# Performance work log

Measured on AMD Instinct MI355X. Metric: run time of the kernel, lower is better.

The kernel has to match this reference:

```python
import jax, jax.numpy as jnp
import numpy as np

NV = 10000
NF = 20000
BATCH = 8


def _make_faces(nv, nf):
    # Synthetic closed-ish mesh connectivity: each vertex touches several faces,
    # guaranteeing every diagonal (degree) entry is > 0.
    i = np.arange(nf)
    half = nf // 2
    f0 = i % nv
    f1 = np.where(i < half, (i + 1) % nv, (i + 3) % nv)
    f2 = np.where(i < half, (i + 2) % nv, (i + 5) % nv)
    return np.stack([f0, f1, f2], axis=1).astype(np.int64)


def _build_laplacian(nv, faces):
    # Faithful replication of LaplacianLoss.__init__ (assignment, not accumulation).
    L = np.zeros((nv, nv), dtype=np.float32)
    f0, f1, f2 = faces[:, 0], faces[:, 1], faces[:, 2]
    L[f0, f1] = -1
    L[f1, f0] = -1
    L[f1, f2] = -1
    L[f2, f1] = -1
    L[f2, f0] = -1
    L[f0, f2] = -1
    r = np.arange(nv)
    L[r, r] = -L.sum(1)  # degree on diagonal
    L /= L[r, r][:, None]  # normalize each row by its diagonal
    return L


def setup_inputs() -> dict:
    key = jax.random.key(0)
    kx, kw = jax.random.split(key)
    faces = _make_faces(NV, NF)
    laplacian = jnp.asarray(_build_laplacian(NV, faces))  # [nv, nv]
    x = jax.random.normal(kx, (BATCH, NV, 3), dtype=jnp.float32)
    vertex_weight = jax.random.uniform(kw, (1,), dtype=jnp.float32) + 0.5
    return {"x": x, "laplacian": laplacian, "vertex_weight": vertex_weight}


def reference(x, laplacian, vertex_weight):
    # lx[b, i, k] = sum_j L[i, j] * x[b, j, k]
    lx = jnp.einsum('ij,bjk->bik', laplacian, x)
    lx = lx * vertex_weight
    # torch.norm over dims (1,2) == Frobenius norm per batch element; scaled by nv
    nv = x.shape[1]
    return jnp.sqrt(jnp.sum(lx * lx, axis=(1, 2))) * nv  # [B]
```

## Files before the change

### kernel.cpp

```cpp
#include <hip/hip_runtime.h>
#include <math.h>


#define NVERT 10000
#define TJ 256
#define NTILES 40
#define TPG 10
#define JG 4
#define RPW 4
#define RPB 16
#define NROWG 625
#define GRID1 (NROWG * JG)
#define GRID2 40

__global__ __launch_bounds__(256, 3) void lap_main(
    const float* __restrict__ x, const float* __restrict__ L,
    float* __restrict__ C) {
  __shared__ __align__(16) float smem[6400];

  const int tid  = threadIdx.x;
  const int lane = tid & 63;
  const int wave = tid >> 6;
  const int rg   = blockIdx.x >> 2;
  const int jg   = blockIdx.x & 3;
  const int row0 = rg * RPB + wave * RPW;

  __align__(16) float acc[RPW][24];
#pragma unroll
  for (int r = 0; r < RPW; ++r)
#pragma unroll
    for (int n = 0; n < 24; ++n) acc[r][n] = 0.f;

  const float4* __restrict__ xg = (const float4*)x;

  for (int tt = 0; tt < TPG; ++tt) {
    const int t = jg * TPG + tt;
    const int jcount = (t == NTILES - 1) ? (NVERT - t * TJ) : TJ;
    __syncthreads();

    const int nf4 = (jcount * 3) >> 2;
    if (tid < nf4) {
#pragma unroll
      for (int b = 0; b < 8; ++b)
        ((float4*)smem)[b * 192 + tid] = xg[b * 7500 + t * 192 + tid];
    }
    __syncthreads();

    const int col0 = t * TJ + 4 * lane;
    if (4 * lane < jcount) {
      __align__(16) float Lv[RPW][4];
#pragma unroll
      for (int r = 0; r < RPW; ++r)
        *(float4*)&Lv[r][0] =
            *(const float4*)(L + (long)(row0 + r) * NVERT + col0);

      const float* xs = smem + 12 * lane;
#pragma unroll
      for (int b = 0; b < 8; ++b) {
        __align__(16) float xv[12];
        *(float4*)&xv[0] = *(const float4*)(xs + b * 768);
        *(float4*)&xv[4] = *(const float4*)(xs + b * 768 + 4);
        *(float4*)&xv[8] = *(const float4*)(xs + b * 768 + 8);
#pragma unroll
        for (int r = 0; r < RPW; ++r)
#pragma unroll
          for (int jj = 0; jj < 4; ++jj)
#pragma unroll
            for (int k = 0; k < 3; ++k)
              acc[r][b * 3 + k] += Lv[r][jj] * xv[jj * 3 + k];
      }
    }
  }

  for (int w = 0; w < 4; ++w) {
    __syncthreads();
    if (wave == w) {
#pragma unroll
      for (int r = 0; r < RPW; ++r)
#pragma unroll
        for (int c = 0; c < 6; ++c)
          *(float4*)&smem[lane * 100 + r * 24 + c * 4] = *(float4*)&acc[r][c * 4];
    }
    __syncthreads();
    if (tid < 96) {
      float s = 0.f;
#pragma unroll
      for (int l = 0; l < 64; ++l) s += smem[l * 100 + tid];
      const int row = rg * RPB + w * RPW + tid / 24;
      atomicAdd(&C[row * 24 + (tid % 24)], s);
    }
  }
}

__global__ __launch_bounds__(256) void lap_reduce(
    const float* __restrict__ C, const float* __restrict__ wv,
    float* __restrict__ out, float* __restrict__ Sg, unsigned* __restrict__ ctr) {
  __shared__ float sS[8];
  const int tid = threadIdx.x;
  if (tid < 8) sS[tid] = 0.f;
  __syncthreads();

  const int row = blockIdx.x * 256 + tid;
  float pb[8] = {0.f, 0.f, 0.f, 0.f, 0.f, 0.f, 0.f, 0.f};
  if (row < NVERT) {
    const float* rp = C + (long)row * 24;
#pragma unroll
    for (int b = 0; b < 8; ++b) {
      float s = 0.f;
#pragma unroll
      for (int k = 0; k < 3; ++k) {
        float v = rp[b * 3 + k];
        s += v * v;
      }
      pb[b] = s;
    }
  }
#pragma unroll
  for (int b = 0; b < 8; ++b) atomicAdd(&sS[b], pb[b]);
  __syncthreads();
  if (tid < 8) atomicAdd(&Sg[tid], sS[tid]);
  __syncthreads();

  if (tid == 0) {
    __threadfence();
    unsigned old = atomicAdd(ctr, 1u);
    if (old == (unsigned)(gridDim.x - 1)) {
      __threadfence();
      const float w = wv[0];
#pragma unroll
      for (int b = 0; b < 8; ++b) {
        float s = atomicAdd(&Sg[b], 0.f);
        out[b] = w * sqrtf(s) * (float)NVERT;
      }
    }
  }
}

extern "C" void kernel_launch(void* const* d_in, const int* in_sizes, int n_in,
                              void* d_out, int out_size, void* d_ws, size_t ws_size,
                              hipStream_t stream) {
  const float* x  = (const float*)d_in[0];
  const float* L  = (const float*)d_in[1];
  const float* wv = (const float*)d_in[2];
  float* out = (float*)d_out;

  float* C       = (float*)d_ws;
  float* Sg      = (float*)((char*)d_ws + 960000);
  unsigned* ctr  = (unsigned*)((char*)d_ws + 960032);

  hipMemsetAsync(d_ws, 0, 960064, stream);
  lap_main<<<GRID1, 256, 0, stream>>>(x, L, C);
  lap_reduce<<<GRID2, 256, 0, stream>>>(C, wv, out, Sg, ctr);
}
```

Before: 630.3 us.

## Read x directly from global memory and prefetch next L tile in registers

Drops the shared-memory staging of x and both block barriers per tile; each lane now loads its x slice straight from global memory (cached in L1/L2). The L tile for the next iteration is prefetched into registers so its load overlaps the FMAs. The partial last tile is handled by a separate scalar tail loop on 16 lanes. The trade-off is redundant global/L1 traffic for x across the four waves, plus extra register pressure from the prefetch buffer.

Result: slower. 1.402 ms (+122.4%).

```diff
diff --git a/kernel.cpp b/kernel.cpp
--- a/kernel.cpp
+++ b/kernel.cpp
@@ -4,7 +4,6 @@
 
 #define NVERT 10000
 #define TJ 256
-#define NTILES 40
 #define TPG 10
 #define JG 4
 #define RPW 4
@@ -31,43 +30,64 @@
 #pragma unroll
     for (int n = 0; n < 24; ++n) acc[r][n] = 0.f;
 
-  const float4* __restrict__ xg = (const float4*)x;
+  const int jbase = jg * (TPG * TJ);
+  const int ntF   = (jg == JG - 1) ? (TPG - 1) : TPG;
 
-  for (int tt = 0; tt < TPG; ++tt) {
-    const int t = jg * TPG + tt;
-    const int jcount = (t == NTILES - 1) ? (NVERT - t * TJ) : TJ;
-    __syncthreads();
+  const float* Lp  = L + (long)row0 * NVERT + jbase + 4 * lane;
+  const float* xp0 = x + (long)(jbase + 4 * lane) * 3;
 
-    const int nf4 = (jcount * 3) >> 2;
-    if (tid < nf4) {
+  __align__(16) float Lv[RPW][4], Ln[RPW][4];
 #pragma unroll
-      for (int b = 0; b < 8; ++b)
-        ((float4*)smem)[b * 192 + tid] = xg[b * 7500 + t * 192 + tid];
-    }
-    __syncthreads();
+  for (int r = 0; r < RPW; ++r)
+    *(float4*)&Lv[r][0] = *(const float4*)(Lp + (long)r * NVERT);
 
-    const int col0 = t * TJ + 4 * lane;
-    if (4 * lane < jcount) {
-      __align__(16) float Lv[RPW][4];
+  for (int t = 0; t < ntF; ++t) {
+    if (t + 1 < ntF) {
 #pragma unroll
       for (int r = 0; r < RPW; ++r)
-        *(float4*)&Lv[r][0] =
-            *(const float4*)(L + (long)(row0 + r) * NVERT + col0);
+        *(float4*)&Ln[r][0] =
+            *(const float4*)(Lp + (long)r * NVERT + (t + 1) * TJ);
+    }
 
-      const float* xs = smem + 12 * lane;
+    const float* xp = xp0 + (long)t * (TJ * 3);
 #pragma unroll
-      for (int b = 0; b < 8; ++b) {
-        __align__(16) float xv[12];
-        *(float4*)&xv[0] = *(const float4*)(xs + b * 768);
-        *(float4*)&xv[4] = *(const float4*)(xs + b * 768 + 4);
-        *(float4*)&xv[8] = *(const float4*)(xs + b * 768 + 8);
+    for (int b = 0; b < 8; ++b) {
+      __align__(16) float xv[12];
+      *(float4*)&xv[0] = *(const float4*)(xp + (long)b * 30000);
+      *(float4*)&xv[4] = *(const float4*)(xp + (long)b * 30000 + 4);
+      *(float4*)&xv[8] = *(const float4*)(xp + (long)b * 30000 + 8);
 #pragma unroll
-        for (int r = 0; r < RPW; ++r)
+      for (int r = 0; r < RPW; ++r)
 #pragma unroll
-          for (int jj = 0; jj < 4; ++jj)
+        for (int jj = 0; jj < 4; ++jj)
 #pragma unroll
-            for (int k = 0; k < 3; ++k)
-              acc[r][b * 3 + k] += Lv[r][jj] * xv[jj * 3 + k];
+          for (int k = 0; k < 3; ++k)
+            acc[r][b * 3 + k] += Lv[r][jj] * xv[jj * 3 + k];
+    }
+
+    if (t + 1 < ntF) {
+#pragma unroll
+      for (int r = 0; r < RPW; ++r)
+#pragma unroll
+        for (int jj = 0; jj < 4; ++jj) Lv[r][jj] = Ln[r][jj];
+    }
+  }
+
+  if (jg == JG - 1 && lane < 16) {
+    const int col = jbase + (TPG - 1) * TJ + lane;
+    float Lt[RPW];
+#pragma unroll
+    for (int r = 0; r < RPW; ++r)
+      Lt[r] = L[(long)(row0 + r) * NVERT + col];
+#pragma unroll
+    for (int b = 0; b < 8; ++b) {
+      const float* xb = x + (long)(b * NVERT + col) * 3;
+      const float x0 = xb[0], x1 = xb[1], x2 = xb[2];
+#pragma unroll
+      for (int r = 0; r < RPW; ++r) {
+        acc[r][b * 3 + 0] += Lt[r] * x0;
+        acc[r][b * 3 + 1] += Lt[r] * x1;
+        acc[r][b * 3 + 2] += Lt[r] * x2;
       }
     }
   }
```
